# Kernel tuning notes

Hardware: AMD Instinct MI355X
Metric: run time of the kernel (lower is better)

The kernel has to match this reference:

```python
import jax, jax.numpy as jnp
import numpy as np

N_ATOM_TYPES = 100
EMBED_DIM = 32
HIDDEN_DIM = 256
B, W, D = 16, 256, 64


def setup_inputs() -> dict:
    key = jax.random.key(0)
    ks = jax.random.split(key, 16)
    inp = {
        "atom1_idx": jax.random.randint(ks[0], (B, W, D), 0, N_ATOM_TYPES),
        "atom2_idx": jax.random.randint(ks[1], (B, W, D), 0, N_ATOM_TYPES),
        "distances": jax.random.uniform(ks[2], (B, W, D), jnp.float32) * 20.0,
        "mask": jax.random.bernoulli(ks[3], 0.9, (B, W, D)),
        # parameters
        "atom_embed": jax.random.normal(ks[4], (N_ATOM_TYPES + 1, EMBED_DIM), jnp.float32) * 0.02,
        "w_in": jax.random.normal(ks[5], (2 * EMBED_DIM + 1, HIDDEN_DIM), jnp.float32) * 0.05,
        "b_in": jnp.zeros((HIDDEN_DIM,), jnp.float32),
        "w_a1": jax.random.normal(ks[6], (HIDDEN_DIM, HIDDEN_DIM // 4), jnp.float32) * 0.05,
        "b_a1": jnp.zeros((HIDDEN_DIM // 4,), jnp.float32),
        "w_a2": jax.random.normal(ks[7], (HIDDEN_DIM // 4, 1), jnp.float32) * 0.05,
        "b_a2": jnp.zeros((1,), jnp.float32),
        "w_v1": jax.random.normal(ks[8], (HIDDEN_DIM, HIDDEN_DIM), jnp.float32) * 0.05,
        "b_v1": jnp.zeros((HIDDEN_DIM,), jnp.float32),
        "w_v2": jax.random.normal(ks[9], (HIDDEN_DIM, HIDDEN_DIM), jnp.float32) * 0.05,
        "b_v2": jnp.zeros((HIDDEN_DIM,), jnp.float32),
        "fallback": jnp.zeros((HIDDEN_DIM,), jnp.float32),
    }
    return inp


def _gelu(x):
    return jax.nn.gelu(x, approximate=False)  # torch default GELU is exact erf form


def reference(atom1_idx, atom2_idx, distances, mask,
              atom_embed, w_in, b_in, w_a1, b_a1, w_a2, b_a2,
              w_v1, b_v1, w_v2, b_v2, fallback):
    # zero padding row (padding_idx = n_atom_types); also kills its grad like torch
    pad = atom_embed.shape[0] - 1
    table = atom_embed * (jnp.arange(atom_embed.shape[0]) != pad)[:, None]
    e1 = table[atom1_idx]                     # [B,W,D,E]
    e2 = table[atom2_idx]                     # [B,W,D,E]
    d = distances * mask.astype(distances.dtype)
    combined = jnp.concatenate([e1, e2, d[..., None]], axis=-1)   # [B,W,D,2E+1]
    hidden = _gelu(combined @ w_in + b_in)    # [B,W,D,H] (dropout = identity in eval)
    scores = (_gelu(hidden @ w_a1 + b_a1) @ w_a2 + b_a2)[..., 0]  # [B,W,D]
    scores = jnp.where(mask, scores, jnp.float32(-10000.0))
    attn = jax.nn.softmax(scores, axis=-1)    # [B,W,D]
    values = _gelu(hidden @ w_v1 + b_v1) @ w_v2 + b_v2            # [B,W,D,H]
    out = jnp.sum(values * attn[..., None], axis=2)               # [B,W,H]
    any_valid = jnp.any(mask, axis=2)
    return jnp.where(any_valid[..., None], out, fallback)
```

## Files before the change

kernel.cpp:

```cpp
#include <hip/hip_runtime.h>
#include <math.h>

#define BW 4096
#define DD 64
#define HH 256

typedef __bf16 bf16x8 __attribute__((ext_vector_type(8)));
typedef float  f32x4  __attribute__((ext_vector_type(4)));
typedef unsigned short u16x8 __attribute__((ext_vector_type(8)));

#define WIN_OFF 0
#define WA1_OFF 16384
#define WV1_OFF 32768
#define WV2_OFF 98304

__device__ __forceinline__ unsigned short to_bf16u(float f) {
    union { __bf16 b; unsigned short u; } cv;
    cv.b = (__bf16)f;
    return cv.u;
}

__device__ __forceinline__ float gelu_fast(float x) {
    float x2 = x * x;
    float z  = x * __builtin_fmaf(-0.10294344f, x2, -2.3022082f);
    float e  = __builtin_amdgcn_exp2f(z);
    return x * __builtin_amdgcn_rcpf(1.0f + e);
}

__device__ __forceinline__ f32x4 mfma16(bf16x8 a, bf16x8 b, f32x4 c) {
    return __builtin_amdgcn_mfma_f32_16x16x32_bf16(a, b, c, 0, 0, 0);
}

__global__ void pack_weights(const float* __restrict__ w_in,
                             const float* __restrict__ w_a1,
                             const float* __restrict__ w_v1,
                             const float* __restrict__ w_v2,
                             unsigned short* __restrict__ ws) {
    int t = blockIdx.x * 256 + threadIdx.x;
    if (t >= 20480) return;
    int lane = t & 63;
    int g = lane >> 4, li = lane & 15;
    u16x8 v;
    if (t < 2048) {
        int fr = t >> 6;
        int kin = fr >> 4, ht = fr & 15;
        #pragma unroll
        for (int j = 0; j < 8; ++j) {
            int k = kin * 32 + 8 * g + j;
            v[j] = to_bf16u(w_in[(size_t)k * 256 + 16 * ht + li]);
        }
        *(u16x8*)(ws + WIN_OFF + (size_t)t * 8) = v;
    } else if (t < 4096) {
        int c = t - 2048;
        int fr = c >> 6;
        int kt = fr >> 2, ct = fr & 3;
        #pragma unroll
        for (int j = 0; j < 8; ++j) {
            int k = kt * 32 + 16 * (j >> 2) + 4 * g + (j & 3);
            v[j] = to_bf16u(w_a1[(size_t)k * 64 + ct * 16 + li]);
        }
        *(u16x8*)(ws + WA1_OFF + (size_t)c * 8) = v;
    } else if (t < 12288) {
        int c = t - 4096;
        int fr = c >> 6;
        int kt = fr >> 4, ct = fr & 15;
        #pragma unroll
        for (int j = 0; j < 8; ++j) {
            int k = kt * 32 + 16 * (j >> 2) + 4 * g + (j & 3);
            v[j] = to_bf16u(w_v1[(size_t)k * 256 + ct * 16 + li]);
        }
        *(u16x8*)(ws + WV1_OFF + (size_t)c * 8) = v;
    } else {
        int c = t - 12288;
        int fr = c >> 6;
        int kt = fr >> 4, ct = fr & 15;
        #pragma unroll
        for (int j = 0; j < 8; ++j) {
            int k = kt * 32 + 8 * g + j;
            v[j] = to_bf16u(w_v2[(size_t)k * 256 + ct * 16 + li]);
        }
        *(u16x8*)(ws + WV2_OFF + (size_t)c * 8) = v;
    }
}

__global__ __launch_bounds__(256, 4)
void dist_attn_kernel(const int*   __restrict__ a1,
                      const int*   __restrict__ a2,
                      const float* __restrict__ dist,
                      const int*   __restrict__ mask,
                      const float* __restrict__ table,
                      const float* __restrict__ w_in,
                      const float* __restrict__ b_in,
                      const float* __restrict__ b_a1,
                      const float* __restrict__ w_a2,
                      const float* __restrict__ b_a2,
                      const float* __restrict__ b_v1,
                      const float* __restrict__ b_v2,
                      const float* __restrict__ fb,
                      const unsigned short* __restrict__ ws,
                      float*       __restrict__ out) {
    __shared__ __align__(16) unsigned char sU[8192];
    __shared__ __align__(16) unsigned short hidfrag[4][8][64][8];

    unsigned short (*combfrag)[2][64][8] = (unsigned short (*)[2][64][8])sU;
    float*          scorep = (float*)sU;
    float*          attn_s = (float*)(sU + 1024);
    unsigned short* r_bf   = (unsigned short*)(sU + 2048);

    const int tid = threadIdx.x;
    const int l   = tid & 63;
    const int w   = tid >> 6;
    const int g   = l >> 4;
    const int li  = l & 15;
    const int blk = blockIdx.x;
    const long base = (long)blk * DD;

    {
        const int i1 = a1[base + 16 * w + li];
        const int i2 = a2[base + 16 * w + li];
        #pragma unroll
        for (int ks = 0; ks < 2; ++ks) {
            const int idx = ks ? i2 : i1;
            const float* srcp = table + (size_t)idx * 32 + 8 * g;
            f32x4 v0 = *(const f32x4*)srcp;
            f32x4 v1 = *(const f32x4*)(srcp + 4);
            u16x8 u;
            #pragma unroll
            for (int j = 0; j < 4; ++j) { u[j] = to_bf16u(v0[j]); u[j + 4] = to_bf16u(v1[j]); }
            *(u16x8*)&combfrag[w][ks][l][0] = u;
        }
    }
    __syncthreads();

    {
        bf16x8 cb[4][2];
        #pragma unroll
        for (int dt = 0; dt < 4; ++dt)
            #pragma unroll
            for (int ks = 0; ks < 2; ++ks)
                cb[dt][ks] = *(const bf16x8*)&combfrag[dt][ks][l][0];
        float dmv[4];
        #pragma unroll
        for (int dt = 0; dt < 4; ++dt) {
            int m = mask[base + 16 * dt + li];
            dmv[dt] = m ? dist[base + 16 * dt + li] : 0.0f;
        }
        #pragma unroll
        for (int hp = 0; hp < 2; ++hp) {
            u16x8 pend[4];
            #pragma unroll
            for (int b = 0; b < 2; ++b) {
                const int ht = 4 * w + 2 * hp + b;
                bf16x8 af0 = *(const bf16x8*)(ws + WIN_OFF + ((size_t)(0 * 16 + ht) * 64 + l) * 8);
                bf16x8 af1 = *(const bf16x8*)(ws + WIN_OFF + ((size_t)(1 * 16 + ht) * 64 + l) * 8);
                f32x4 w64v = *(const f32x4*)&w_in[64 * 256 + 16 * ht + 4 * g];
                f32x4 binv = *(const f32x4*)&b_in[16 * ht + 4 * g];
                #pragma unroll
                for (int dt = 0; dt < 4; ++dt) {
                    f32x4 acc;
                    #pragma unroll
                    for (int p = 0; p < 4; ++p)
                        acc[p] = __builtin_fmaf(dmv[dt], w64v[p], binv[p]);
                    acc = mfma16(af0, cb[dt][0], acc);
                    acc = mfma16(af1, cb[dt][1], acc);
                    #pragma unroll
                    for (int p = 0; p < 4; ++p)
                        pend[dt][4 * b + p] = to_bf16u(gelu_fast(acc[p]));
                }
            }
            #pragma unroll
            for (int dt = 0; dt < 4; ++dt)
                *(u16x8*)&hidfrag[dt][2 * w + hp][l][0] = pend[dt];
        }
    }
    __syncthreads();

    {
        bf16x8 ba[8];
        #pragma unroll
        for (int kt = 0; kt < 8; ++kt)
            ba[kt] = *(const bf16x8*)(ws + WA1_OFF + ((size_t)(kt * 4 + w) * 64 + l) * 8);
        f32x4 acc2[4];
        #pragma unroll
        for (int rt = 0; rt < 4; ++rt) acc2[rt] = (f32x4){0.f, 0.f, 0.f, 0.f};
        #pragma unroll
        for (int kt = 0; kt < 8; ++kt) {
            #pragma unroll
            for (int rt = 0; rt < 4; ++rt) {
                bf16x8 a = *(const bf16x8*)&hidfrag[rt][kt][l][0];
                acc2[rt] = mfma16(a, ba[kt], acc2[rt]);
            }
        }
        const float ba1 = b_a1[16 * w + li];
        const float wa2 = w_a2[16 * w + li];
        #pragma unroll
        for (int rt = 0; rt < 4; ++rt) {
            float s[4];
            #pragma unroll
            for (int p = 0; p < 4; ++p) s[p] = gelu_fast(acc2[rt][p] + ba1) * wa2;
            #pragma unroll
            for (int off = 1; off <= 8; off <<= 1)
                #pragma unroll
                for (int p = 0; p < 4; ++p) s[p] += __shfl_xor(s[p], off, 64);
            if (li == 0) {
                f32x4 sv; sv[0] = s[0]; sv[1] = s[1]; sv[2] = s[2]; sv[3] = s[3];
                *(f32x4*)&scorep[w * 64 + 16 * rt + 4 * g] = sv;
            }
        }
    }
    __syncthreads();

    {
        const int m = mask[base + l];
        float sc = scorep[l] + scorep[64 + l] + scorep[128 + l] + scorep[192 + l] + b_a2[0];
        if (!m) sc = -10000.0f;
        float mx = sc;
        #pragma unroll
        for (int off = 32; off; off >>= 1) mx = fmaxf(mx, __shfl_xor(mx, off, 64));
        float p = __expf(sc - mx);
        float sm = p;
        #pragma unroll
        for (int off = 32; off; off >>= 1) sm += __shfl_xor(sm, off, 64);
        attn_s[w * 64 + l] = p / sm;
    }

    {
        f32x4 av[4];
        #pragma unroll
        for (int rt = 0; rt < 4; ++rt) av[rt] = *(const f32x4*)&attn_s[w * 64 + 16 * rt + 4 * g];
        #pragma unroll
        for (int half = 0; half < 2; ++half) {
            f32x4 acc3[2][4];
            #pragma unroll
            for (int c2 = 0; c2 < 2; ++c2)
                #pragma unroll
                for (int rt = 0; rt < 4; ++rt) acc3[c2][rt] = (f32x4){0.f, 0.f, 0.f, 0.f};
            #pragma unroll
            for (int kt = 0; kt < 8; ++kt) {
                bf16x8 b0 = *(const bf16x8*)(ws + WV1_OFF + ((size_t)(kt * 16 + 4 * w + 2 * half + 0) * 64 + l) * 8);
                bf16x8 b1 = *(const bf16x8*)(ws + WV1_OFF + ((size_t)(kt * 16 + 4 * w + 2 * half + 1) * 64 + l) * 8);
                bf16x8 a[4];
                #pragma unroll
                for (int rt = 0; rt < 4; ++rt) a[rt] = *(const bf16x8*)&hidfrag[rt][kt][l][0];
                #pragma unroll
                for (int rt = 0; rt < 4; ++rt) {
                    acc3[0][rt] = mfma16(a[rt], b0, acc3[0][rt]);
                    acc3[1][rt] = mfma16(a[rt], b1, acc3[1][rt]);
                }
            }
            #pragma unroll
            for (int c2 = 0; c2 < 2; ++c2) {
                const int ct = 2 * half + c2;
                const int c = 64 * w + 16 * ct + li;
                const float bv = b_v1[c];
                float val = 0.f;
                #pragma unroll
                for (int rt = 0; rt < 4; ++rt)
                    #pragma unroll
                    for (int p = 0; p < 4; ++p)
                        val += av[rt][p] * gelu_fast(acc3[c2][rt][p] + bv);
                val += __shfl_xor(val, 16, 64);
                val += __shfl_xor(val, 32, 64);
                if (g == 0) r_bf[c] = to_bf16u(val);
            }
        }
    }
    __syncthreads();

    {
        const int anyv = __any(mask[base + l] != 0);
        f32x4 acc[4];
        #pragma unroll
        for (int ct = 0; ct < 4; ++ct) acc[ct] = (f32x4){0.f, 0.f, 0.f, 0.f};
        #pragma unroll
        for (int kt = 0; kt < 8; ++kt) {
            bf16x8 a = *(const bf16x8*)&r_bf[kt * 32 + 8 * g];
            #pragma unroll
            for (int ct = 0; ct < 4; ++ct) {
                bf16x8 b = *(const bf16x8*)(ws + WV2_OFF + ((size_t)(kt * 16 + 4 * w + ct) * 64 + l) * 8);
                acc[ct] = mfma16(a, b, acc[ct]);
            }
        }
        if (g == 0) {
            #pragma unroll
            for (int ct = 0; ct < 4; ++ct) {
                const int c = 16 * (4 * w + ct) + li;
                float o = acc[ct][0] + b_v2[c];
                if (!anyv) o = fb[c];
                out[(size_t)blk * HH + c] = o;
            }
        }
    }
}

extern "C" void kernel_launch(void* const* d_in, const int* in_sizes, int n_in,
                              void* d_out, int out_size, void* d_ws, size_t ws_size,
                              hipStream_t stream) {
    const int*   a1    = (const int*)  d_in[0];
    const int*   a2    = (const int*)  d_in[1];
    const float* dist  = (const float*)d_in[2];
    const int*   mask  = (const int*)  d_in[3];
    const float* table = (const float*)d_in[4];
    const float* w_in  = (const float*)d_in[5];
    const float* b_in  = (const float*)d_in[6];
    const float* w_a1  = (const float*)d_in[7];
    const float* b_a1  = (const float*)d_in[8];
    const float* w_a2  = (const float*)d_in[9];
    const float* b_a2  = (const float*)d_in[10];
    const float* w_v1  = (const float*)d_in[11];
    const float* b_v1  = (const float*)d_in[12];
    const float* w_v2  = (const float*)d_in[13];
    const float* b_v2  = (const float*)d_in[14];
    const float* fb    = (const float*)d_in[15];
    float* out = (float*)d_out;
    unsigned short* ws = (unsigned short*)d_ws;

    pack_weights<<<80, 256, 0, stream>>>(w_in, w_a1, w_v1, w_v2, ws);
    dist_attn_kernel<<<BW, 256, 0, stream>>>(a1, a2, dist, mask, table,
                                             w_in, b_in, b_a1, w_a2, b_a2,
                                             b_v1, b_v2, fb, ws, out);
}
```

Measured before the change: 101.0 us.

## Process two (b,w) positions per block to reuse weight fragments

Each block now handles two positions instead of one, so every weight fragment loaded from global memory feeds MFMAs for both positions. Grid size is halved, and LDS grows to about 69 KB for the per-position hidden fragments, scores and reduced values. Launch bounds drop to 2 blocks per CU, trading occupancy and register headroom for fewer weight loads per unit of work. An extra barrier is added after the combined fragments are read, because they now alias the hidden-fragment buffer.

Result: slower. 109.8 us (+8.7%).

```diff
diff --git a/kernel.cpp b/kernel.cpp
--- a/kernel.cpp
+++ b/kernel.cpp
@@ -4,6 +4,7 @@
 #define BW 4096
 #define DD 64
 #define HH 256
+#define NPOS 2
 
 typedef __bf16 bf16x8 __attribute__((ext_vector_type(8)));
 typedef float  f32x4  __attribute__((ext_vector_type(4)));
@@ -83,7 +84,7 @@
     }
 }
 
-__global__ __launch_bounds__(256, 4)
+__global__ __launch_bounds__(256, 2)
 void dist_attn_kernel(const int*   __restrict__ a1,
                       const int*   __restrict__ a2,
                       const float* __restrict__ dist,
@@ -99,25 +100,27 @@
                       const float* __restrict__ fb,
                       const unsigned short* __restrict__ ws,
                       float*       __restrict__ out) {
-    __shared__ __align__(16) unsigned char sU[8192];
-    __shared__ __align__(16) unsigned short hidfrag[4][8][64][8];
-
-    unsigned short (*combfrag)[2][64][8] = (unsigned short (*)[2][64][8])sU;
-    float*          scorep = (float*)sU;
-    float*          attn_s = (float*)(sU + 1024);
-    unsigned short* r_bf   = (unsigned short*)(sU + 2048);
+    __shared__ __align__(16) unsigned char lds[70656];
+    unsigned short (*hidfrag)[4][8][64][8]  = (unsigned short (*)[4][8][64][8])lds;
+    unsigned short (*combfrag)[4][2][64][8] = (unsigned short (*)[4][2][64][8])lds;
+    float*          scorep = (float*)(lds + 65536);
+    float*          attn_s = (float*)(lds + 67584);
+    unsigned short* r_bf   = (unsigned short*)(lds + 69632);
 
     const int tid = threadIdx.x;
     const int l   = tid & 63;
     const int w   = tid >> 6;
     const int g   = l >> 4;
     const int li  = l & 15;
-    const int blk = blockIdx.x;
-    const long base = (long)blk * DD;
-
-    {
-        const int i1 = a1[base + 16 * w + li];
-        const int i2 = a2[base + 16 * w + li];
+    long base[NPOS];
+    #pragma unroll
+    for (int pos = 0; pos < NPOS; ++pos)
+        base[pos] = ((long)blockIdx.x * NPOS + pos) * DD;
+
+    #pragma unroll
+    for (int pos = 0; pos < NPOS; ++pos) {
+        const int i1 = a1[base[pos] + 16 * w + li];
+        const int i2 = a2[base[pos] + 16 * w + li];
         #pragma unroll
         for (int ks = 0; ks < 2; ++ks) {
             const int idx = ks ? i2 : i1;
@@ -127,27 +130,33 @@
             u16x8 u;
             #pragma unroll
             for (int j = 0; j < 4; ++j) { u[j] = to_bf16u(v0[j]); u[j + 4] = to_bf16u(v1[j]); }
-            *(u16x8*)&combfrag[w][ks][l][0] = u;
+            *(u16x8*)&combfrag[pos][w][ks][l][0] = u;
         }
     }
     __syncthreads();
 
     {
-        bf16x8 cb[4][2];
-        #pragma unroll
-        for (int dt = 0; dt < 4; ++dt)
-            #pragma unroll
-            for (int ks = 0; ks < 2; ++ks)
-                cb[dt][ks] = *(const bf16x8*)&combfrag[dt][ks][l][0];
-        float dmv[4];
-        #pragma unroll
-        for (int dt = 0; dt < 4; ++dt) {
-            int m = mask[base + 16 * dt + li];
-            dmv[dt] = m ? dist[base + 16 * dt + li] : 0.0f;
-        }
+        bf16x8 cb[NPOS][4][2];
+        #pragma unroll
+        for (int pos = 0; pos < NPOS; ++pos)
+            #pragma unroll
+            for (int dt = 0; dt < 4; ++dt)
+                #pragma unroll
+                for (int ks = 0; ks < 2; ++ks)
+                    cb[pos][dt][ks] = *(const bf16x8*)&combfrag[pos][dt][ks][l][0];
+        float dmv[NPOS][4];
+        #pragma unroll
+        for (int pos = 0; pos < NPOS; ++pos)
+            #pragma unroll
+            for (int dt = 0; dt < 4; ++dt) {
+                int m = mask[base[pos] + 16 * dt + li];
+                dmv[pos][dt] = m ? dist[base[pos] + 16 * dt + li] : 0.0f;
+            }
+        __syncthreads();
+
         #pragma unroll
         for (int hp = 0; hp < 2; ++hp) {
-            u16x8 pend[4];
+            u16x8 pend[NPOS][4];
             #pragma unroll
             for (int b = 0; b < 2; ++b) {
                 const int ht = 4 * w + 2 * hp + b;
@@ -156,21 +165,26 @@
                 f32x4 w64v = *(const f32x4*)&w_in[64 * 256 + 16 * ht + 4 * g];
                 f32x4 binv = *(const f32x4*)&b_in[16 * ht + 4 * g];
                 #pragma unroll
-                for (int dt = 0; dt < 4; ++dt) {
-                    f32x4 acc;
-                    #pragma unroll
-                    for (int p = 0; p < 4; ++p)
-                        acc[p] = __builtin_fmaf(dmv[dt], w64v[p], binv[p]);
-                    acc = mfma16(af0, cb[dt][0], acc);
-                    acc = mfma16(af1, cb[dt][1], acc);
-                    #pragma unroll
-                    for (int p = 0; p < 4; ++p)
-                        pend[dt][4 * b + p] = to_bf16u(gelu_fast(acc[p]));
-                }
-            }
-            #pragma unroll
-            for (int dt = 0; dt < 4; ++dt)
-                *(u16x8*)&hidfrag[dt][2 * w + hp][l][0] = pend[dt];
+                for (int pos = 0; pos < NPOS; ++pos) {
+                    #pragma unroll
+                    for (int dt = 0; dt < 4; ++dt) {
+                        f32x4 acc;
+                        #pragma unroll
+                        for (int p = 0; p < 4; ++p)
+                            acc[p] = __builtin_fmaf(dmv[pos][dt], w64v[p], binv[p]);
+                        acc = mfma16(af0, cb[pos][dt][0], acc);
+                        acc = mfma16(af1, cb[pos][dt][1], acc);
+                        #pragma unroll
+                        for (int p = 0; p < 4; ++p)
+                            pend[pos][dt][4 * b + p] = to_bf16u(gelu_fast(acc[p]));
+                    }
+                }
+            }
+            #pragma unroll
+            for (int pos = 0; pos < NPOS; ++pos)
+                #pragma unroll
+                for (int dt = 0; dt < 4; ++dt)
+                    *(u16x8*)&hidfrag[pos][dt][2 * w + hp][l][0] = pend[pos][dt];
         }
     }
     __syncthreads();
@@ -180,39 +194,47 @@
         #pragma unroll
         for (int kt = 0; kt < 8; ++kt)
             ba[kt] = *(const bf16x8*)(ws + WA1_OFF + ((size_t)(kt * 4 + w) * 64 + l) * 8);
-        f32x4 acc2[4];
-        #pragma unroll
-        for (int rt = 0; rt < 4; ++rt) acc2[rt] = (f32x4){0.f, 0.f, 0.f, 0.f};
+        f32x4 acc2[NPOS][4];
+        #pragma unroll
+        for (int pos = 0; pos < NPOS; ++pos)
+            #pragma unroll
+            for (int rt = 0; rt < 4; ++rt) acc2[pos][rt] = (f32x4){0.f, 0.f, 0.f, 0.f};
         #pragma unroll
         for (int kt = 0; kt < 8; ++kt) {
             #pragma unroll
-            for (int rt = 0; rt < 4; ++rt) {
-                bf16x8 a = *(const bf16x8*)&hidfrag[rt][kt][l][0];
-                acc2[rt] = mfma16(a, ba[kt], acc2[rt]);
-            }
+            for (int pos = 0; pos < NPOS; ++pos)
+                #pragma unroll
+                for (int rt = 0; rt < 4; ++rt) {
+                    bf16x8 a = *(const bf16x8*)&hidfrag[pos][rt][kt][l][0];
+                    acc2[pos][rt] = mfma16(a, ba[kt], acc2[pos][rt]);
+                }
         }
         const float ba1 = b_a1[16 * w + li];
         const float wa2 = w_a2[16 * w + li];
         #pragma unroll
-        for (int rt = 0; rt < 4; ++rt) {
-            float s[4];
-            #pragma unroll
-            for (int p = 0; p < 4; ++p) s[p] = gelu_fast(acc2[rt][p] + ba1) * wa2;
-            #pragma unroll
-            for (int off = 1; off <= 8; off <<= 1)
-                #pragma unroll
-                for (int p = 0; p < 4; ++p) s[p] += __shfl_xor(s[p], off, 64);
-            if (li == 0) {
-                f32x4 sv; sv[0] = s[0]; sv[1] = s[1]; sv[2] = s[2]; sv[3] = s[3];
-                *(f32x4*)&scorep[w * 64 + 16 * rt + 4 * g] = sv;
-            }
-        }
+        for (int pos = 0; pos < NPOS; ++pos)
+            #pragma unroll
+            for (int rt = 0; rt < 4; ++rt) {
+                float s[4];
+                #pragma unroll
+                for (int p = 0; p < 4; ++p) s[p] = gelu_fast(acc2[pos][rt][p] + ba1) * wa2;
+                #pragma unroll
+                for (int off = 1; off <= 8; off <<= 1)
+                    #pragma unroll
+                    for (int p = 0; p < 4; ++p) s[p] += __shfl_xor(s[p], off, 64);
+                if (li == 0) {
+                    f32x4 sv; sv[0] = s[0]; sv[1] = s[1]; sv[2] = s[2]; sv[3] = s[3];
+                    *(f32x4*)&scorep[pos * 256 + w * 64 + 16 * rt + 4 * g] = sv;
+                }
+            }
     }
     __syncthreads();
 
-    {
-        const int m = mask[base + l];
-        float sc = scorep[l] + scorep[64 + l] + scorep[128 + l] + scorep[192 + l] + b_a2[0];
+    #pragma unroll
+    for (int pos = 0; pos < NPOS; ++pos) {
+        const int m = mask[base[pos] + l];
+        const float* sp = scorep + pos * 256;
+        float sc = sp[l] + sp[64 + l] + sp[128 + l] + sp[192 + l] + b_a2[0];
         if (!m) sc = -10000.0f;
         float mx = sc;
         #pragma unroll
@@ -221,74 +243,96 @@
         float sm = p;
         #pragma unroll
         for (int off = 32; off; off >>= 1) sm += __shfl_xor(sm, off, 64);
-        attn_s[w * 64 + l] = p / sm;
+        attn_s[pos * 256 + w * 64 + l] = p / sm;
     }
 
     {
-        f32x4 av[4];
-        #pragma unroll
-        for (int rt = 0; rt < 4; ++rt) av[rt] = *(const f32x4*)&attn_s[w * 64 + 16 * rt + 4 * g];
+        f32x4 av[NPOS][4];
+        #pragma unroll
+        for (int pos = 0; pos < NPOS; ++pos)
+            #pragma unroll
+            for (int rt = 0; rt < 4; ++rt)
+                av[pos][rt] = *(const f32x4*)&attn_s[pos * 256 + w * 64 + 16 * rt + 4 * g];
         #pragma unroll
         for (int half = 0; half < 2; ++half) {
-            f32x4 acc3[2][4];
-            #pragma unroll
-            for (int c2 = 0; c2 < 2; ++c2)
-                #pragma unroll
-                for (int rt = 0; rt < 4; ++rt) acc3[c2][rt] = (f32x4){0.f, 0.f, 0.f, 0.f};
+            f32x4 acc3[NPOS][2][4];
+            #pragma unroll
+            for (int pos = 0; pos < NPOS; ++pos)
+                #pragma unroll
+                for (int c2 = 0; c2 < 2; ++c2)
+                    #pragma unroll
+                    for (int rt = 0; rt < 4; ++rt) acc3[pos][c2][rt] = (f32x4){0.f, 0.f, 0.f, 0.f};
             #pragma unroll
             for (int kt = 0; kt < 8; ++kt) {
                 bf16x8 b0 = *(const bf16x8*)(ws + WV1_OFF + ((size_t)(kt * 16 + 4 * w + 2 * half + 0) * 64 + l) * 8);
                 bf16x8 b1 = *(const bf16x8*)(ws + WV1_OFF + ((size_t)(kt * 16 + 4 * w + 2 * half + 1) * 64 + l) * 8);
-                bf16x8 a[4];
-                #pragma unroll
-                for (int rt = 0; rt < 4; ++rt) a[rt] = *(const bf16x8*)&hidfrag[rt][kt][l][0];
-                #pragma unroll
-                for (int rt = 0; rt < 4; ++rt) {
-                    acc3[0][rt] = mfma16(a[rt], b0, acc3[0][rt]);
-                    acc3[1][rt] = mfma16(a[rt], b1, acc3[1][rt]);
-                }
-            }
-            #pragma unroll
-            for (int c2 = 0; c2 < 2; ++c2) {
-                const int ct = 2 * half + c2;
-                const int c = 64 * w + 16 * ct + li;
-                const float bv = b_v1[c];
-                float val = 0.f;
-                #pragma unroll
-                for (int rt = 0; rt < 4; ++rt)
-                    #pragma unroll
-                    for (int p = 0; p < 4; ++p)
-                        val += av[rt][p] * gelu_fast(acc3[c2][rt][p] + bv);
-                val += __shfl_xor(val, 16, 64);
-                val += __shfl_xor(val, 32, 64);
-                if (g == 0) r_bf[c] = to_bf16u(val);
-            }
+                #pragma unroll
+                for (int pos = 0; pos < NPOS; ++pos) {
+                    bf16x8 a[4];
+                    #pragma unroll
+                    for (int rt = 0; rt < 4; ++rt) a[rt] = *(const bf16x8*)&hidfrag[pos][rt][kt][l][0];
+                    #pragma unroll
+                    for (int rt = 0; rt < 4; ++rt) {
+                        acc3[pos][0][rt] = mfma16(a[rt], b0, acc3[pos][0][rt]);
+                        acc3[pos][1][rt] = mfma16(a[rt], b1, acc3[pos][1][rt]);
+                    }
+                }
+            }
+            #pragma unroll
+            for (int pos = 0; pos < NPOS; ++pos)
+                #pragma unroll
+                for (int c2 = 0; c2 < 2; ++c2) {
+                    const int ct = 2 * half + c2;
+                    const int c = 64 * w + 16 * ct + li;
+                    const float bv = b_v1[c];
+                    float val = 0.f;
+                    #pragma unroll
+                    for (int rt = 0; rt < 4; ++rt)
+                        #pragma unroll
+                        for (int p = 0; p < 4; ++p)
+                            val += av[pos][rt][p] * gelu_fast(acc3[pos][c2][rt][p] + bv);
+                    val += __shfl_xor(val, 16, 64);
+                    val += __shfl_xor(val, 32, 64);
+                    if (g == 0) r_bf[pos * 256 + c] = to_bf16u(val);
+                }
         }
     }
     __syncthreads();
 
     {
-        const int anyv = __any(mask[base + l] != 0);
-        f32x4 acc[4];
-        #pragma unroll
-        for (int ct = 0; ct < 4; ++ct) acc[ct] = (f32x4){0.f, 0.f, 0.f, 0.f};
+        int anyv[NPOS];
+        #pragma unroll
+        for (int pos = 0; pos < NPOS; ++pos)
+            anyv[pos] = __any(mask[base[pos] + l] != 0);
+        f32x4 acc[NPOS][4];
+        #pragma unroll
+        for (int pos = 0; pos < NPOS; ++pos)
+            #pragma unroll
+            for (int ct = 0; ct < 4; ++ct) acc[pos][ct] = (f32x4){0.f, 0.f, 0.f, 0.f};
         #pragma unroll
         for (int kt = 0; kt < 8; ++kt) {
-            bf16x8 a = *(const bf16x8*)&r_bf[kt * 32 + 8 * g];
+            bf16x8 a[NPOS];
+            #pragma unroll
+            for (int pos = 0; pos < NPOS; ++pos)
+                a[pos] = *(const bf16x8*)&r_bf[pos * 256 + kt * 32 + 8 * g];
             #pragma unroll
             for (int ct = 0; ct < 4; ++ct) {
                 bf16x8 b = *(const bf16x8*)(ws + WV2_OFF + ((size_t)(kt * 16 + 4 * w + ct) * 64 + l) * 8);
-                acc[ct] = mfma16(a, b, acc[ct]);
+                #pragma unroll
+                for (int pos = 0; pos < NPOS; ++pos)
+                    acc[pos][ct] = mfma16(a[pos], b, acc[pos][ct]);
             }
         }
         if (g == 0) {
             #pragma unroll
-            for (int ct = 0; ct < 4; ++ct) {
-                const int c = 16 * (4 * w + ct) + li;
-                float o = acc[ct][0] + b_v2[c];
-                if (!anyv) o = fb[c];
-                out[(size_t)blk * HH + c] = o;
-            }
+            for (int pos = 0; pos < NPOS; ++pos)
+                #pragma unroll
+                for (int ct = 0; ct < 4; ++ct) {
+                    const int c = 16 * (4 * w + ct) + li;
+                    float o = acc[pos][ct][0] + b_v2[c];
+                    if (!anyv[pos]) o = fb[c];
+                    out[(base[pos] / DD) * (size_t)HH + c] = o;
+                }
         }
     }
 }
@@ -316,7 +360,7 @@
     unsigned short* ws = (unsigned short*)d_ws;
 
     pack_weights<<<80, 256, 0, stream>>>(w_in, w_a1, w_v1, w_v2, ws);
-    dist_attn_kernel<<<BW, 256, 0, stream>>>(a1, a2, dist, mask, table,
-                                             w_in, b_in, b_a1, w_a2, b_a2,
-                                             b_v1, b_v2, fb, ws, out);
-}
+    dist_attn_kernel<<<BW / NPOS, 256, 0, stream>>>(a1, a2, dist, mask, table,
+                                                    w_in, b_in, b_a1, w_a2, b_a2,
+                                                    b_v1, b_v2, fb, ws, out);
+}
```
